# Performance work log

Measured on AMD Instinct MI355X. Metric: run time of the kernel, lower is better.

Reference implementation:

```python
import jax, jax.numpy as jnp
import numpy as np

B = 16384            # rays per chunk
NUM_BINS = 129       # num_samples + 1 fenceposts
RESAMPLE_PADDING = 0.01


def setup_inputs() -> dict:
    key = jax.random.key(0)
    k1, k2, k3, k4, k5 = jax.random.split(key, 5)
    origins = jax.random.normal(k1, (B, 3), dtype=jnp.float32)
    d = jax.random.normal(k2, (B, 3), dtype=jnp.float32)
    directions = d / jnp.linalg.norm(d, axis=-1, keepdims=True)
    radii = jax.random.uniform(k3, (B, 1), dtype=jnp.float32, minval=0.001, maxval=0.005)
    # sorted fencepost distances in [near=2, far=6]
    t_vals = jnp.sort(jax.random.uniform(k4, (B, NUM_BINS), dtype=jnp.float32, minval=2.0, maxval=6.0), axis=-1)
    weights = jax.random.uniform(k5, (B, NUM_BINS - 1), dtype=jnp.float32)
    return dict(origins=origins, directions=directions, radii=radii, t_vals=t_vals, weights=weights)


def _piecewise_constant_pdf(bins, weights, num_samples):
    """Inverse-CDF sampling (randomized=False). Math identical to the torch
    mask/max/min formulation: searchsorted(cdf, u, 'right') gives the first
    index with cdf > u (the min over ~mask), and idx-1 the last index with
    cdf <= u (the max over mask); u in [0, 1-eps) so indices are in range."""
    eps = 1e-5
    wsum = jnp.sum(weights, axis=-1, keepdims=True)
    pad = jnp.maximum(0.0, eps - wsum)
    weights = weights + pad / weights.shape[-1]
    wsum = wsum + pad
    pdf = weights / wsum
    cdf = jnp.minimum(1.0, jnp.cumsum(pdf[..., :-1], axis=-1))
    cdf = jnp.concatenate([jnp.zeros_like(cdf[..., :1]), cdf, jnp.ones_like(cdf[..., :1])], axis=-1)  # [B, bins]
    u = jnp.linspace(0.0, 1.0 - jnp.finfo(jnp.float32).eps, num_samples, dtype=jnp.float32)
    u = jnp.broadcast_to(u, cdf.shape[:-1] + (num_samples,))
    idx1 = jax.vmap(lambda c, uu: jnp.searchsorted(c, uu, side='right'))(cdf, u)
    idx1 = jnp.clip(idx1, 1, cdf.shape[-1] - 1)
    idx0 = idx1 - 1
    take = lambda x, i: jnp.take_along_axis(x, i, axis=-1)
    bins_g0, bins_g1 = take(bins, idx0), take(bins, idx1)
    cdf_g0, cdf_g1 = take(cdf, idx0), take(cdf, idx1)
    t = jnp.clip(jnp.nan_to_num((u - cdf_g0) / (cdf_g1 - cdf_g0), nan=0.0), 0.0, 1.0)
    return bins_g0 + t * (bins_g1 - bins_g0)


def _conical_frustum_to_gaussian(d, t0, t1, base_radius):
    """Stable cone->Gaussian (diag covariance), lifted along ray axis d."""
    mu = (t0 + t1) / 2
    hw = (t1 - t0) / 2
    denom = 3 * mu ** 2 + hw ** 2
    t_mean = mu + 2 * mu * hw ** 2 / denom
    t_var = hw ** 2 / 3 - 4 / 15 * (hw ** 4 * (12 * mu ** 2 - hw ** 2) / denom ** 2)
    r_var = base_radius ** 2 * (mu ** 2 / 4 + 5 / 12 * hw ** 2 - 4 / 15 * hw ** 4 / denom)
    mean = d[..., None, :] * t_mean[..., None]                       # [B, S, 3]
    d_mag_sq = jnp.sum(d ** 2, axis=-1, keepdims=True) + 1e-10
    d_outer_diag = d ** 2
    null_outer_diag = 1 - d_outer_diag / d_mag_sq
    cov_diag = t_var[..., None] * d_outer_diag[..., None, :] + r_var[..., None] * null_outer_diag[..., None, :]
    return mean, cov_diag


def reference(origins, directions, radii, t_vals, weights):
    # blur weights (max-pool then avg of neighbors) + padding
    wpad = jnp.concatenate([weights[..., :1], weights, weights[..., -1:]], axis=-1)
    wmax = jnp.maximum(wpad[..., :-1], wpad[..., 1:])
    wblur = 0.5 * (wmax[..., :-1] + wmax[..., 1:])
    w = wblur + RESAMPLE_PADDING
    # stop_grad=True in the torch module (torch.no_grad around resampling)
    new_t_vals = jax.lax.stop_gradient(_piecewise_constant_pdf(t_vals, w, t_vals.shape[-1]))
    t0, t1 = new_t_vals[..., :-1], new_t_vals[..., 1:]
    means, covs = _conical_frustum_to_gaussian(directions, t0, t1, radii)
    means = means + origins[..., None, :]
    return new_t_vals, means, covs
```

## Files before the change

kernel.cpp:

```cpp
#include <hip/hip_runtime.h>

#define NRAYS 16384
#define NB 129
#define NW 128

__global__ __launch_bounds__(256) void mipnerf_inv_kernel(
    const float* __restrict__ origins,
    const float* __restrict__ directions,
    const float* __restrict__ radii,
    const float* __restrict__ t_vals,
    const float* __restrict__ weights,
    float* __restrict__ out_t,
    float* __restrict__ out_means,
    float* __restrict__ out_covs)
{
    __shared__ __align__(16) float s_t  [4 * NB];
    __shared__ __align__(16) float s_w  [4 * NW];
    __shared__ __align__(16) float s_nt [4 * NB];
    __shared__ __align__(16) float s_mean[4 * NW * 3];
    __shared__ __align__(16) float s_cov [4 * NW * 3];

    const int tid = threadIdx.x;
    const int wv  = tid >> 6;
    const int l   = tid & 63;
    const int blk = blockIdx.x;
    const int ray = (blk << 2) + wv;

    if (tid < NB)
        reinterpret_cast<float4*>(s_t)[tid] =
            reinterpret_cast<const float4*>(t_vals + (long)blk * (4 * NB))[tid];
    if (tid < NW)
        reinterpret_cast<float4*>(s_w)[tid] =
            reinterpret_cast<const float4*>(weights + (long)blk * (4 * NW))[tid];
    __syncthreads();

    const float* wrow = s_w + wv * NW;
    const float w0  = wrow[2 * l];
    const float w1  = wrow[2 * l + 1];
    const float wm1 = (l == 0)  ? w0 : wrow[2 * l - 1];
    const float wp1 = (l == 63) ? w1 : wrow[2 * l + 2];

    const float mx01 = fmaxf(w0, w1);
    const float wb0 = 0.5f * (fmaxf(wm1, w0) + mx01) + 0.01f;
    const float wb1 = 0.5f * (mx01 + fmaxf(w1, wp1)) + 0.01f;

    float S = wb0 + wb1;
    #pragma unroll
    for (int off = 1; off < 64; off <<= 1) {
        const float t = __shfl_up(S, off);
        if (l >= off) S += t;
    }
    const float W1 = S;
    const float W0 = S - wb1;
    const float inv_wsum = 1.0f / __shfl(S, 63);

    const float c_lo  = (l == 0)  ? 0.0f : fminf(1.0f, (W0 - wb0) * inv_wsum);
    const float c_mid = fminf(1.0f, W0 * inv_wsum);
    const float c_hi  = (l == 63) ? 1.0f : fminf(1.0f, W1 * inv_wsum);

    const float* bins = s_t + wv * NB;
    const float b0 = bins[2 * l];
    const float b1 = bins[2 * l + 1];
    const float b2 = bins[2 * l + 2];

    const float ueps     = 1.0f - 1.1920929e-7f;
    const float step     = ueps / 128.0f;
    const float inv_step = 128.0f / ueps;
    const int s0 = (int)ceilf(c_lo  * inv_step);
    const int s1 = (int)ceilf(c_mid * inv_step);
    const int s2 = (int)ceilf(c_hi  * inv_step);

    float* ntrow = s_nt + wv * NB;
    {
        const float inv_d = 1.0f / (c_mid - c_lo);
        const float db = b1 - b0;
        for (int s = s0; s < s1; ++s) {
            float tt = ((float)s * step - c_lo) * inv_d;
            tt = fminf(fmaxf(tt, 0.0f), 1.0f);
            ntrow[s] = fmaf(tt, db, b0);
        }
    }
    {
        const float inv_d = 1.0f / (c_hi - c_mid);
        const float db = b2 - b1;
        for (int s = s1; s < s2; ++s) {
            float tt = ((float)s * step - c_mid) * inv_d;
            tt = fminf(fmaxf(tt, 0.0f), 1.0f);
            ntrow[s] = fmaf(tt, db, b1);
        }
    }
    __builtin_amdgcn_wave_barrier();

    const float n0 = ntrow[2 * l];
    const float n1 = ntrow[2 * l + 1];
    const float n2 = ntrow[2 * l + 2];

    const float dx = directions[ray * 3 + 0];
    const float dy = directions[ray * 3 + 1];
    const float dz = directions[ray * 3 + 2];
    const float ox = origins[ray * 3 + 0];
    const float oy = origins[ray * 3 + 1];
    const float oz = origins[ray * 3 + 2];
    const float rad = radii[ray];
    const float rad2 = rad * rad;
    const float dx2 = dx * dx, dy2 = dy * dy, dz2 = dz * dz;
    const float inv_dms = 1.0f / (dx2 + dy2 + dz2 + 1e-10f);
    const float nullx = 1.0f - dx2 * inv_dms;
    const float nully = 1.0f - dy2 * inv_dms;
    const float nullz = 1.0f - dz2 * inv_dms;

    float* mrow = s_mean + wv * (NW * 3) + 6 * l;
    float* crow = s_cov  + wv * (NW * 3) + 6 * l;
    const float tt0[2] = { n0, n1 };
    const float tt1[2] = { n1, n2 };
    #pragma unroll
    for (int k = 0; k < 2; ++k) {
        const float mu = 0.5f * (tt0[k] + tt1[k]);
        const float hw = 0.5f * (tt1[k] - tt0[k]);
        const float mu2 = mu * mu, hw2 = hw * hw;
        const float inv_denom = 1.0f / (3.0f * mu2 + hw2);
        const float t_mean = mu + 2.0f * mu * hw2 * inv_denom;
        const float t_var  = hw2 * (1.0f / 3.0f)
                           - (4.0f / 15.0f) * (hw2 * hw2 * (12.0f * mu2 - hw2) * inv_denom * inv_denom);
        const float r_var  = rad2 * (0.25f * mu2 + (5.0f / 12.0f) * hw2
                                     - (4.0f / 15.0f) * hw2 * hw2 * inv_denom);
        mrow[3 * k + 0] = fmaf(dx, t_mean, ox);
        mrow[3 * k + 1] = fmaf(dy, t_mean, oy);
        mrow[3 * k + 2] = fmaf(dz, t_mean, oz);
        crow[3 * k + 0] = fmaf(t_var, dx2, r_var * nullx);
        crow[3 * k + 1] = fmaf(t_var, dy2, r_var * nully);
        crow[3 * k + 2] = fmaf(t_var, dz2, r_var * nullz);
    }
    __syncthreads();

    if (tid < NB)
        reinterpret_cast<float4*>(out_t + (long)blk * (4 * NB))[tid] =
            reinterpret_cast<const float4*>(s_nt)[tid];

    float4* om4 = reinterpret_cast<float4*>(out_means + (long)blk * (4 * NW * 3));
    float4* oc4 = reinterpret_cast<float4*>(out_covs  + (long)blk * (4 * NW * 3));
    const float4* sm4 = reinterpret_cast<const float4*>(s_mean);
    const float4* sc4 = reinterpret_cast<const float4*>(s_cov);
    #pragma unroll
    for (int i = tid; i < 4 * NW * 3 / 4; i += 256) {
        om4[i] = sm4[i];
        oc4[i] = sc4[i];
    }
}

extern "C" void kernel_launch(void* const* d_in, const int* in_sizes, int n_in,
                              void* d_out, int out_size, void* d_ws, size_t ws_size,
                              hipStream_t stream) {
    const float* origins    = (const float*)d_in[0];
    const float* directions = (const float*)d_in[1];
    const float* radii      = (const float*)d_in[2];
    const float* t_vals     = (const float*)d_in[3];
    const float* weights    = (const float*)d_in[4];

    float* out_t     = (float*)d_out;
    float* out_means = out_t + (long)NRAYS * NB;
    float* out_covs  = out_means + (long)NRAYS * NW * 3;

    const int grid = NRAYS / 4;
    mipnerf_inv_kernel<<<grid, 256, 0, stream>>>(
        origins, directions, radii, t_vals, weights, out_t, out_means, out_covs);
}
```

Baseline: 19.56 us.

## Make each wave independent: direct global loads, shuffles, wave-local stores

Each wave now loads its own ray's weights and t_vals straight from global memory and gets neighbour weights through lane shuffles, so the shared-memory staging of inputs goes away. Both block-wide __syncthreads are replaced by wave barriers, and each wave writes its own outputs, so the four waves in a block no longer wait on each other. Direction, origin and radius loads are moved earlier to overlap with the scan. In exchange, t_vals loads become strided scalar loads and out_t is stored as scalar rows instead of float4, which may hurt coalescing.

```diff
diff --git a/kernel.cpp b/kernel.cpp
--- a/kernel.cpp
+++ b/kernel.cpp
@@ -4,7 +4,7 @@
 #define NB 129
 #define NW 128
 
-__global__ __launch_bounds__(256) void mipnerf_inv_kernel(
+__global__ __launch_bounds__(256) void mipnerf_waveind_kernel(
     const float* __restrict__ origins,
     const float* __restrict__ directions,
     const float* __restrict__ radii,
@@ -14,32 +14,32 @@
     float* __restrict__ out_means,
     float* __restrict__ out_covs)
 {
-    __shared__ __align__(16) float s_t  [4 * NB];
-    __shared__ __align__(16) float s_w  [4 * NW];
-    __shared__ __align__(16) float s_nt [4 * NB];
-    __shared__ __align__(16) float s_mean[4 * NW * 3];
-    __shared__ __align__(16) float s_cov [4 * NW * 3];
+    __shared__ __align__(16) float s_nt  [4][NB + 3];
+    __shared__ __align__(16) float s_mean[4][NW * 3];
+    __shared__ __align__(16) float s_cov [4][NW * 3];
 
     const int tid = threadIdx.x;
     const int wv  = tid >> 6;
     const int l   = tid & 63;
-    const int blk = blockIdx.x;
-    const int ray = (blk << 2) + wv;
+    const int ray = (blockIdx.x << 2) + wv;
 
-    if (tid < NB)
-        reinterpret_cast<float4*>(s_t)[tid] =
-            reinterpret_cast<const float4*>(t_vals + (long)blk * (4 * NB))[tid];
-    if (tid < NW)
-        reinterpret_cast<float4*>(s_w)[tid] =
-            reinterpret_cast<const float4*>(weights + (long)blk * (4 * NW))[tid];
-    __syncthreads();
+    const float2 wp = *reinterpret_cast<const float2*>(weights + (long)ray * NW + 2 * l);
+    const float w0 = wp.x, w1 = wp.y;
+    const float* trow = t_vals + (long)ray * NB;
+    const float b0 = trow[2 * l];
+    const float b1 = trow[2 * l + 1];
+    const float b2 = trow[2 * l + 2];
 
-    const float* wrow = s_w + wv * NW;
-    const float w0  = wrow[2 * l];
-    const float w1  = wrow[2 * l + 1];
-    const float wm1 = (l == 0)  ? w0 : wrow[2 * l - 1];
-    const float wp1 = (l == 63) ? w1 : wrow[2 * l + 2];
+    const float dx = directions[ray * 3 + 0];
+    const float dy = directions[ray * 3 + 1];
+    const float dz = directions[ray * 3 + 2];
+    const float ox = origins[ray * 3 + 0];
+    const float oy = origins[ray * 3 + 1];
+    const float oz = origins[ray * 3 + 2];
+    const float rad = radii[ray];
 
+    float wm1 = __shfl_up(w1, 1);   if (l == 0)  wm1 = w0;
+    float wp1 = __shfl_down(w0, 1); if (l == 63) wp1 = w1;
     const float mx01 = fmaxf(w0, w1);
     const float wb0 = 0.5f * (fmaxf(wm1, w0) + mx01) + 0.01f;
     const float wb1 = 0.5f * (mx01 + fmaxf(w1, wp1)) + 0.01f;
@@ -58,11 +58,6 @@
     const float c_mid = fminf(1.0f, W0 * inv_wsum);
     const float c_hi  = (l == 63) ? 1.0f : fminf(1.0f, W1 * inv_wsum);
 
-    const float* bins = s_t + wv * NB;
-    const float b0 = bins[2 * l];
-    const float b1 = bins[2 * l + 1];
-    const float b2 = bins[2 * l + 2];
-
     const float ueps     = 1.0f - 1.1920929e-7f;
     const float step     = ueps / 128.0f;
     const float inv_step = 128.0f / ueps;
@@ -70,7 +65,7 @@
     const int s1 = (int)ceilf(c_mid * inv_step);
     const int s2 = (int)ceilf(c_hi  * inv_step);
 
-    float* ntrow = s_nt + wv * NB;
+    float* ntrow = s_nt[wv];
     {
         const float inv_d = 1.0f / (c_mid - c_lo);
         const float db = b1 - b0;
@@ -95,13 +90,6 @@
     const float n1 = ntrow[2 * l + 1];
     const float n2 = ntrow[2 * l + 2];
 
-    const float dx = directions[ray * 3 + 0];
-    const float dy = directions[ray * 3 + 1];
-    const float dz = directions[ray * 3 + 2];
-    const float ox = origins[ray * 3 + 0];
-    const float oy = origins[ray * 3 + 1];
-    const float oz = origins[ray * 3 + 2];
-    const float rad = radii[ray];
     const float rad2 = rad * rad;
     const float dx2 = dx * dx, dy2 = dy * dy, dz2 = dz * dz;
     const float inv_dms = 1.0f / (dx2 + dy2 + dz2 + 1e-10f);
@@ -109,8 +97,8 @@
     const float nully = 1.0f - dy2 * inv_dms;
     const float nullz = 1.0f - dz2 * inv_dms;
 
-    float* mrow = s_mean + wv * (NW * 3) + 6 * l;
-    float* crow = s_cov  + wv * (NW * 3) + 6 * l;
+    float* mrow = s_mean[wv] + 6 * l;
+    float* crow = s_cov[wv]  + 6 * l;
     const float tt0[2] = { n0, n1 };
     const float tt1[2] = { n1, n2 };
     #pragma unroll
@@ -131,20 +119,22 @@
         crow[3 * k + 1] = fmaf(t_var, dy2, r_var * nully);
         crow[3 * k + 2] = fmaf(t_var, dz2, r_var * nullz);
     }
-    __syncthreads();
+    __builtin_amdgcn_wave_barrier();
 
-    if (tid < NB)
-        reinterpret_cast<float4*>(out_t + (long)blk * (4 * NB))[tid] =
-            reinterpret_cast<const float4*>(s_nt)[tid];
+    float* po = out_t + (long)ray * NB;
+    po[l]      = ntrow[l];
+    po[64 + l] = ntrow[64 + l];
+    if (l == 0) po[128] = ntrow[128];
 
-    float4* om4 = reinterpret_cast<float4*>(out_means + (long)blk * (4 * NW * 3));
-    float4* oc4 = reinterpret_cast<float4*>(out_covs  + (long)blk * (4 * NW * 3));
-    const float4* sm4 = reinterpret_cast<const float4*>(s_mean);
-    const float4* sc4 = reinterpret_cast<const float4*>(s_cov);
-    #pragma unroll
-    for (int i = tid; i < 4 * NW * 3 / 4; i += 256) {
-        om4[i] = sm4[i];
-        oc4[i] = sc4[i];
+    float4* pm = reinterpret_cast<float4*>(out_means + (long)ray * (NW * 3));
+    float4* pc = reinterpret_cast<float4*>(out_covs  + (long)ray * (NW * 3));
+    const float4* sm = reinterpret_cast<const float4*>(s_mean[wv]);
+    const float4* sc = reinterpret_cast<const float4*>(s_cov[wv]);
+    pm[l] = sm[l];
+    pc[l] = sc[l];
+    if (l < 32) {
+        pm[64 + l] = sm[64 + l];
+        pc[64 + l] = sc[64 + l];
     }
 }
 
@@ -162,6 +152,6 @@
     float* out_covs  = out_means + (long)NRAYS * NW * 3;
 
     const int grid = NRAYS / 4;
-    mipnerf_inv_kernel<<<grid, 256, 0, stream>>>(
+    mipnerf_waveind_kernel<<<grid, 256, 0, stream>>>(
         origins, directions, radii, t_vals, weights, out_t, out_means, out_covs);
 }
```

Result: no change. 19.28 us (-1.4%).
